# Kernel optimization log

Hardware: AMD Instinct MI355X
Metric: run time of the kernel (lower is better)

The kernel has to match this reference:

```python
import jax, jax.numpy as jnp
import numpy as np


def _lstm_scan(x_seq, W_ih, W_hh, b_ih, b_hh, hidden):
    # x_seq: [T, E]; returns final h: [1, H]. PyTorch LSTMCell gate order: i, f, g, o.
    H = hidden
    b = b_ih + b_hh  # fuse biases once

    def step(carry, x_t):
        h, c = carry  # [1, H] each
        gates = x_t[None, :] @ W_ih.T + h @ W_hh.T + b  # [1, 4H]
        i = jax.nn.sigmoid(gates[:, 0 * H:1 * H])
        f = jax.nn.sigmoid(gates[:, 1 * H:2 * H])
        g = jnp.tanh(gates[:, 2 * H:3 * H])
        o = jax.nn.sigmoid(gates[:, 3 * H:4 * H])
        c = f * c + i * g
        h = o * jnp.tanh(c)
        return (h, c), None

    h0 = jnp.zeros((1, H), dtype=x_seq.dtype)
    c0 = jnp.zeros((1, H), dtype=x_seq.dtype)
    (h, _), _ = jax.lax.scan(step, (h0, c0), x_seq)
    return h


def setup_inputs() -> dict:
    key = jax.random.key(0)
    ks = jax.random.split(key, 20)
    V_T, V_A, E, H = 50000, 20000, 1024, 2048
    T_T, T_A = 128, 16
    s = 0.02
    return {
        "x_title": jax.random.randint(ks[0], (T_T,), 0, V_T, dtype=jnp.int64) if jax.config.jax_enable_x64 else jax.random.randint(ks[0], (T_T,), 0, V_T, dtype=jnp.int32),
        "x_authors": jax.random.randint(ks[1], (T_A,), 0, V_A, dtype=jnp.int32),
        "emb_title": jax.random.normal(ks[2], (V_T, E), jnp.float32) * s,
        "emb_authors": jax.random.normal(ks[3], (V_A, E), jnp.float32) * s,
        "W_ih_t": jax.random.normal(ks[4], (4 * H, E), jnp.float32) * s,
        "W_hh_t": jax.random.normal(ks[5], (4 * H, H), jnp.float32) * s,
        "b_ih_t": jax.random.normal(ks[6], (4 * H,), jnp.float32) * s,
        "b_hh_t": jax.random.normal(ks[7], (4 * H,), jnp.float32) * s,
        "W_ih_a": jax.random.normal(ks[8], (4 * H, E), jnp.float32) * s,
        "W_hh_a": jax.random.normal(ks[9], (4 * H, H), jnp.float32) * s,
        "b_ih_a": jax.random.normal(ks[10], (4 * H,), jnp.float32) * s,
        "b_hh_a": jax.random.normal(ks[11], (4 * H,), jnp.float32) * s,
        "W1": jax.random.normal(ks[12], (H, 2 * H), jnp.float32) * s,
        "b1": jax.random.normal(ks[13], (H,), jnp.float32) * s,
        "W2": jax.random.normal(ks[14], (H, H), jnp.float32) * s,
        "b2": jax.random.normal(ks[15], (H,), jnp.float32) * s,
        "W3": jax.random.normal(ks[16], (2, H), jnp.float32) * s,
        "b3": jax.random.normal(ks[17], (2,), jnp.float32) * s,
    }


def reference(x_title, x_authors, emb_title, emb_authors,
              W_ih_t, W_hh_t, b_ih_t, b_hh_t,
              W_ih_a, W_hh_a, b_ih_a, b_hh_a,
              W1, b1, W2, b2, W3, b3):
    H = W_hh_t.shape[1]
    xt = emb_title[x_title]        # [T_t, E]
    xa = emb_authors[x_authors]    # [T_a, E]
    summary_title = _lstm_scan(xt, W_ih_t, W_hh_t, b_ih_t, b_hh_t, H)    # [1, H]
    summary_authors = _lstm_scan(xa, W_ih_a, W_hh_a, b_ih_a, b_hh_a, H)  # [1, H]
    summary = jnp.concatenate([summary_title, summary_authors], axis=1)  # [1, 2H]
    h1 = jax.nn.relu(summary @ W1.T + b1)
    h2 = jax.nn.relu(h1 @ W2.T + b2)
    logit = h2 @ W3.T + b3  # [1, 2]
    return logit
```

## Files before the change

kernel.cpp:

```cpp
#include <hip/hip_runtime.h>
#include <stdint.h>

#define NB 256
typedef unsigned long long u64;

__device__ __forceinline__ float sigm(float x) {
    return 1.f / (1.f + __expf(-x));
}
__device__ __forceinline__ float tanh_fast(float x) {
    return 1.f - 2.f / (__expf(2.f * x) + 1.f);
}

__device__ __forceinline__ u64 aload(u64* p) {
    return __hip_atomic_load(p, __ATOMIC_RELAXED, __HIP_MEMORY_SCOPE_AGENT);
}
__device__ __forceinline__ void astore(u64* p, u64 v) {
    __hip_atomic_store(p, v, __ATOMIC_RELAXED, __HIP_MEMORY_SCOPE_AGENT);
}
__device__ __forceinline__ void poll4(u64* m, unsigned tag, float* dst) {
    u64 v0, v1, v2, v3;
    for (;;) {
        v0 = aload(m + 0);
        v1 = aload(m + 1);
        v2 = aload(m + 2);
        v3 = aload(m + 3);
        if ((unsigned)(v0 >> 32) == tag && (unsigned)(v1 >> 32) == tag &&
            (unsigned)(v2 >> 32) == tag && (unsigned)(v3 >> 32) == tag)
            break;
        __builtin_amdgcn_s_sleep(1);
    }
    dst[0] = __uint_as_float((unsigned)v0);
    dst[1] = __uint_as_float((unsigned)v1);
    dst[2] = __uint_as_float((unsigned)v2);
    dst[3] = __uint_as_float((unsigned)v3);
}

template <int TT>
__global__ __launch_bounds__(256) void gates_x_gemm(
    const int* __restrict__ idx, const float* __restrict__ emb,
    const float* __restrict__ Wih, const float* __restrict__ bih,
    const float* __restrict__ bhh, float* __restrict__ Gx) {
    __shared__ float As[TT][36];
    __shared__ float Ws[32][68];
    const int tid = threadIdx.x;
    const int jt = blockIdx.x * 64;
    const int t0 = blockIdx.y * TT;
    constexpr int TPT = TT / 16;
    const int tx = tid & 15, ty = tid >> 4;
    float acc[TPT][4];
#pragma unroll
    for (int a = 0; a < TPT; ++a)
#pragma unroll
        for (int q = 0; q < 4; ++q) acc[a][q] = 0.f;

    for (int k0 = 0; k0 < 1024; k0 += 32) {
        if constexpr (TT == 32) {
            int t = tid >> 3, kq = (tid & 7) * 4;
            int row = idx[t0 + t];
            float4 v = *(const float4*)(emb + (size_t)row * 1024 + k0 + kq);
            *(float4*)&As[t][kq] = v;
        } else {
            int t = tid >> 4, kq = (tid & 15) * 2;
            int row = idx[t0 + t];
            float2 v = *(const float2*)(emb + (size_t)row * 1024 + k0 + kq);
            *(float2*)&As[t][kq] = v;
        }
        {
            int j = tid >> 3, kq = (tid & 7) * 4;
            float4 w0 = *(const float4*)(Wih + (size_t)(jt + j) * 1024 + k0 + kq);
            float4 w1 = *(const float4*)(Wih + (size_t)(jt + j + 32) * 1024 + k0 + kq);
            const float* p0 = (const float*)&w0;
            const float* p1 = (const float*)&w1;
#pragma unroll
            for (int c = 0; c < 4; ++c) {
                Ws[kq + c][j] = p0[c];
                Ws[kq + c][j + 32] = p1[c];
            }
        }
        __syncthreads();
#pragma unroll
        for (int kk = 0; kk < 32; kk += 4) {
            float4 av[TPT];
#pragma unroll
            for (int tt = 0; tt < TPT; ++tt)
                av[tt] = *(float4*)&As[ty * TPT + tt][kk];
#pragma unroll
            for (int c = 0; c < 4; ++c) {
                float4 wv = *(float4*)&Ws[kk + c][tx * 4];
#pragma unroll
                for (int tt = 0; tt < TPT; ++tt) {
                    const float* ap = (const float*)&av[tt];
                    float a = ap[c];
                    acc[tt][0] += a * wv.x;
                    acc[tt][1] += a * wv.y;
                    acc[tt][2] += a * wv.z;
                    acc[tt][3] += a * wv.w;
                }
            }
        }
        __syncthreads();
    }
    int j = jt + tx * 4;
    float4 bi = *(const float4*)(bih + j);
    float4 bh = *(const float4*)(bhh + j);
#pragma unroll
    for (int tt = 0; tt < TPT; ++tt) {
        int t = t0 + ty * TPT + tt;
        float4 r;
        r.x = acc[tt][0] + bi.x + bh.x;
        r.y = acc[tt][1] + bi.y + bh.y;
        r.z = acc[tt][2] + bi.z + bh.z;
        r.w = acc[tt][3] + bi.w + bh.w;
        *(float4*)(Gx + (size_t)t * 8192 + j) = r;
    }
}

__global__ __launch_bounds__(512, 2) void lstm_mlp_persistent(
    const float* __restrict__ Whh_t, const float* __restrict__ Whh_a,
    const float* __restrict__ Gxt, const float* __restrict__ Gxa,
    const float* __restrict__ W1, const float* __restrict__ b1,
    const float* __restrict__ W2, const float* __restrict__ b2,
    const float* __restrict__ W3, const float* __restrict__ b3,
    u64* msg_t, u64* msg_a, float* out) {
    __shared__ float h_lds[21504];
    __shared__ float part_final[32];
    __shared__ float gsum[32];
    __shared__ float cl[8];
    const int tid = threadIdx.x;
    const int b = blockIdx.x;
    const int w = tid >> 6, l = tid & 63;

    for (int scan = 0; scan < 2; ++scan) {
        const float* Whh = scan ? Whh_a : Whh_t;
        const float* Gx = scan ? Gxa : Gxt;
        u64* msg = scan ? msg_a : msg_t;
        const int T = scan ? 16 : 128;

        float4 wreg[4][8];
#pragma unroll
        for (int r = 0; r < 4; ++r) {
            const int rl = w * 4 + r;
            const int j = (rl >> 3) * 2048 + b * 8 + (rl & 7);
            const float* wrow = Whh + (size_t)j * 2048 + l * 4;
#pragma unroll
            for (int q = 0; q < 8; ++q) wreg[r][q] = *(const float4*)(wrow + q * 256);
        }
        if (tid < 8) cl[tid] = 0.f;

        for (int t = 0; t < T; ++t) {
            float gx;
            if (tid < 32)
                gx = Gx[(size_t)t * 8192 + (tid >> 3) * 2048 + b * 8 + (tid & 7)];
            if (t == 0) {
                *(float4*)(h_lds + tid * 4) = float4{0.f, 0.f, 0.f, 0.f};
            } else {
                poll4(msg + (t & 1) * 2048 + tid * 4, (unsigned)t, h_lds + tid * 4);
            }
            __syncthreads();
            float4 hreg[8];
#pragma unroll
            for (int q = 0; q < 8; ++q) hreg[q] = *(float4*)(h_lds + q * 256 + l * 4);
            float acc[4];
#pragma unroll
            for (int r = 0; r < 4; ++r) {
                float a = 0.f;
#pragma unroll
                for (int q = 0; q < 8; ++q) {
                    a += wreg[r][q].x * hreg[q].x;
                    a += wreg[r][q].y * hreg[q].y;
                    a += wreg[r][q].z * hreg[q].z;
                    a += wreg[r][q].w * hreg[q].w;
                }
                acc[r] = a;
            }
#pragma unroll
            for (int r = 0; r < 4; ++r) {
                float a = acc[r];
#pragma unroll
                for (int off = 32; off; off >>= 1) a += __shfl_xor(a, off, 64);
                if (l == 0) part_final[w * 4 + r] = a;
            }
            __syncthreads();
            if (tid < 32) gsum[tid] = part_final[tid] + gx;
            if (tid < 8) {
                float si = sigm(gsum[tid]);
                float sf = sigm(gsum[8 + tid]);
                float tg = tanh_fast(gsum[16 + tid]);
                float so = sigm(gsum[24 + tid]);
                float c = sf * cl[tid] + si * tg;
                cl[tid] = c;
                float hval = so * tanh_fast(c);
                astore(msg + ((t + 1) & 1) * 2048 + b * 8 + tid,
                       ((u64)(unsigned)(t + 1) << 32) | (u64)__float_as_uint(hval));
            }
        }
    }

    poll4(msg_t + tid * 4, 128u, h_lds + tid * 4);
    poll4(msg_a + tid * 4, 16u, h_lds + 2048 + tid * 4);
    __syncthreads();
    {
        const int j = b * 8 + w;
        const float* wr = W1 + (size_t)j * 4096;
        float acc = 0.f;
#pragma unroll
        for (int i = 0; i < 16; ++i) {
            float4 wv = *(const float4*)(wr + i * 256 + l * 4);
            float4 hv = *(const float4*)(h_lds + i * 256 + l * 4);
            acc += wv.x * hv.x + wv.y * hv.y + wv.z * hv.z + wv.w * hv.w;
        }
#pragma unroll
        for (int off = 32; off; off >>= 1) acc += __shfl_xor(acc, off, 64);
        if (l == 0) {
            float h1 = fmaxf(acc + b1[j], 0.f);
            astore(msg_t + 2048 + j, (129ull << 32) | (u64)__float_as_uint(h1));
        }
    }
    __syncthreads();
    poll4(msg_t + 2048 + tid * 4, 129u, h_lds + tid * 4);
    __syncthreads();
    {
        const int j = b * 8 + w;
        const float* wr = W2 + (size_t)j * 2048;
        float acc = 0.f;
#pragma unroll
        for (int i = 0; i < 8; ++i) {
            float4 wv = *(const float4*)(wr + i * 256 + l * 4);
            float4 hv = *(const float4*)(h_lds + i * 256 + l * 4);
            acc += wv.x * hv.x + wv.y * hv.y + wv.z * hv.z + wv.w * hv.w;
        }
#pragma unroll
        for (int off = 32; off; off >>= 1) acc += __shfl_xor(acc, off, 64);
        if (l == 0) {
            float h2 = fmaxf(acc + b2[j], 0.f);
            astore(msg_t + j, (130ull << 32) | (u64)__float_as_uint(h2));
        }
    }
    if (b == 0) {
        __syncthreads();
        poll4(msg_t + tid * 4, 130u, h_lds + tid * 4);
        __syncthreads();
        if (w < 2) {
            const float* wr = W3 + (size_t)w * 2048;
            float acc = 0.f;
#pragma unroll
            for (int i = 0; i < 8; ++i) {
                float4 wv = *(const float4*)(wr + i * 256 + l * 4);
                float4 hv = *(const float4*)(h_lds + i * 256 + l * 4);
                acc += wv.x * hv.x + wv.y * hv.y + wv.z * hv.z + wv.w * hv.w;
            }
#pragma unroll
            for (int off = 32; off; off >>= 1) acc += __shfl_xor(acc, off, 64);
            if (l == 0) out[w] = acc + b3[w];
        }
    }
}

extern "C" void kernel_launch(void* const* d_in, const int* in_sizes, int n_in,
                              void* d_out, int out_size, void* d_ws,
                              size_t ws_size, hipStream_t stream) {
    const int* x_t = (const int*)d_in[0];
    const int* x_a = (const int*)d_in[1];
    const float* emb_t = (const float*)d_in[2];
    const float* emb_a = (const float*)d_in[3];
    const float* Wih_t = (const float*)d_in[4];
    const float* Whh_t = (const float*)d_in[5];
    const float* bih_t = (const float*)d_in[6];
    const float* bhh_t = (const float*)d_in[7];
    const float* Wih_a = (const float*)d_in[8];
    const float* Whh_a = (const float*)d_in[9];
    const float* bih_a = (const float*)d_in[10];
    const float* bhh_a = (const float*)d_in[11];
    const float* W1 = (const float*)d_in[12];
    const float* b1 = (const float*)d_in[13];
    const float* W2 = (const float*)d_in[14];
    const float* b2 = (const float*)d_in[15];
    const float* W3 = (const float*)d_in[16];
    const float* b3 = (const float*)d_in[17];

    u64* msg_t = (u64*)d_ws;
    u64* msg_a = (u64*)((char*)d_ws + 32768);
    float* gxt = (float*)((char*)d_ws + 65536);
    float* gxa = (float*)((char*)d_ws + 65536 + 4194304);

    hipMemsetAsync(d_ws, 0, 65536, stream);
    gates_x_gemm<32><<<dim3(128, 4), 256, 0, stream>>>(x_t, emb_t, Wih_t, bih_t,
                                                       bhh_t, gxt);
    gates_x_gemm<16><<<dim3(128, 1), 256, 0, stream>>>(x_a, emb_a, Wih_a, bih_a,
                                                       bhh_a, gxa);
    lstm_mlp_persistent<<<NB, 512, 0, stream>>>(Whh_t, Whh_a, gxt, gxa, W1, b1,
                                                W2, b2, W3, b3, msg_t, msg_a,
                                                (float*)d_out);
}
```

Baseline: 1.200 ms.

## Map each warp to one hidden unit's four gates and drop second barrier

Row assignment now gives each wavefront the i, f, g and o rows for one hidden unit. The gate nonlinearity and cell update run in registers right after the shuffle reduction, so the per-step LDS staging and the second __syncthreads go away. The h buffer in LDS is double-buffered by step parity so the next step's poll cannot overwrite values still being read. Polling now uses two 128-bit global loads through inline asm with cache-bypass bits instead of four 64-bit atomic loads. This shortens the serial critical path per timestep, at the cost of relying on the sc0/sc1 asm for coherence and of doing redundant transcendental work across all lanes.

After: 1.163 ms. 3.0% less time.

```diff
diff --git a/kernel.cpp b/kernel.cpp
--- a/kernel.cpp
+++ b/kernel.cpp
@@ -3,6 +3,7 @@
 
 #define NB 256
 typedef unsigned long long u64;
+typedef unsigned uint4v __attribute__((ext_vector_type(4)));
 
 __device__ __forceinline__ float sigm(float x) {
     return 1.f / (1.f + __expf(-x));
@@ -11,28 +12,27 @@
     return 1.f - 2.f / (__expf(2.f * x) + 1.f);
 }
 
-__device__ __forceinline__ u64 aload(u64* p) {
-    return __hip_atomic_load(p, __ATOMIC_RELAXED, __HIP_MEMORY_SCOPE_AGENT);
-}
 __device__ __forceinline__ void astore(u64* p, u64 v) {
     __hip_atomic_store(p, v, __ATOMIC_RELAXED, __HIP_MEMORY_SCOPE_AGENT);
 }
-__device__ __forceinline__ void poll4(u64* m, unsigned tag, float* dst) {
-    u64 v0, v1, v2, v3;
+
+__device__ __forceinline__ void poll4v(const u64* m, unsigned tag, float* dst) {
+    uint4v x, y;
     for (;;) {
-        v0 = aload(m + 0);
-        v1 = aload(m + 1);
-        v2 = aload(m + 2);
-        v3 = aload(m + 3);
-        if ((unsigned)(v0 >> 32) == tag && (unsigned)(v1 >> 32) == tag &&
-            (unsigned)(v2 >> 32) == tag && (unsigned)(v3 >> 32) == tag)
-            break;
+        asm volatile(
+            "global_load_dwordx4 %0, %2, off sc0 sc1\n\t"
+            "global_load_dwordx4 %1, %3, off sc0 sc1\n\t"
+            "s_waitcnt vmcnt(0)"
+            : "=&v"(x), "=&v"(y)
+            : "v"(m), "v"(m + 2)
+            : "memory");
+        if (x.y == tag && x.w == tag && y.y == tag && y.w == tag) break;
         __builtin_amdgcn_s_sleep(1);
     }
-    dst[0] = __uint_as_float((unsigned)v0);
-    dst[1] = __uint_as_float((unsigned)v1);
-    dst[2] = __uint_as_float((unsigned)v2);
-    dst[3] = __uint_as_float((unsigned)v3);
+    dst[0] = __uint_as_float(x.x);
+    dst[1] = __uint_as_float(x.z);
+    dst[2] = __uint_as_float(y.x);
+    dst[3] = __uint_as_float(y.z);
 }
 
 template <int TT>
@@ -123,9 +123,6 @@
     const float* __restrict__ W3, const float* __restrict__ b3,
     u64* msg_t, u64* msg_a, float* out) {
     __shared__ float h_lds[21504];
-    __shared__ float part_final[32];
-    __shared__ float gsum[32];
-    __shared__ float cl[8];
     const int tid = threadIdx.x;
     const int b = blockIdx.x;
     const int w = tid >> 6, l = tid & 63;
@@ -138,66 +135,66 @@
 
         float4 wreg[4][8];
 #pragma unroll
-        for (int r = 0; r < 4; ++r) {
-            const int rl = w * 4 + r;
-            const int j = (rl >> 3) * 2048 + b * 8 + (rl & 7);
+        for (int q = 0; q < 4; ++q) {
+            const int j = q * 2048 + b * 8 + w;
             const float* wrow = Whh + (size_t)j * 2048 + l * 4;
 #pragma unroll
-            for (int q = 0; q < 8; ++q) wreg[r][q] = *(const float4*)(wrow + q * 256);
-        }
-        if (tid < 8) cl[tid] = 0.f;
+            for (int k8 = 0; k8 < 8; ++k8)
+                wreg[q][k8] = *(const float4*)(wrow + k8 * 256);
+        }
+        float c = 0.f;
 
         for (int t = 0; t < T; ++t) {
-            float gx;
-            if (tid < 32)
-                gx = Gx[(size_t)t * 8192 + (tid >> 3) * 2048 + b * 8 + (tid & 7)];
+            float gxv[4];
+#pragma unroll
+            for (int q = 0; q < 4; ++q)
+                gxv[q] = Gx[(size_t)t * 8192 + q * 2048 + b * 8 + w];
+            float* hstage = h_lds + (t & 1) * 2048;
             if (t == 0) {
-                *(float4*)(h_lds + tid * 4) = float4{0.f, 0.f, 0.f, 0.f};
+                *(float4*)(hstage + tid * 4) = float4{0.f, 0.f, 0.f, 0.f};
             } else {
-                poll4(msg + (t & 1) * 2048 + tid * 4, (unsigned)t, h_lds + tid * 4);
+                poll4v(msg + (t & 1) * 2048 + tid * 4, (unsigned)t,
+                       hstage + tid * 4);
             }
             __syncthreads();
             float4 hreg[8];
 #pragma unroll
-            for (int q = 0; q < 8; ++q) hreg[q] = *(float4*)(h_lds + q * 256 + l * 4);
+            for (int k8 = 0; k8 < 8; ++k8)
+                hreg[k8] = *(float4*)(hstage + k8 * 256 + l * 4);
             float acc[4];
 #pragma unroll
-            for (int r = 0; r < 4; ++r) {
+            for (int q = 0; q < 4; ++q) {
                 float a = 0.f;
 #pragma unroll
-                for (int q = 0; q < 8; ++q) {
-                    a += wreg[r][q].x * hreg[q].x;
-                    a += wreg[r][q].y * hreg[q].y;
-                    a += wreg[r][q].z * hreg[q].z;
-                    a += wreg[r][q].w * hreg[q].w;
+                for (int k8 = 0; k8 < 8; ++k8) {
+                    a += wreg[q][k8].x * hreg[k8].x;
+                    a += wreg[q][k8].y * hreg[k8].y;
+                    a += wreg[q][k8].z * hreg[k8].z;
+                    a += wreg[q][k8].w * hreg[k8].w;
                 }
-                acc[r] = a;
-            }
-#pragma unroll
-            for (int r = 0; r < 4; ++r) {
-                float a = acc[r];
+                acc[q] = a;
+            }
+#pragma unroll
+            for (int q = 0; q < 4; ++q) {
+                float a = acc[q];
 #pragma unroll
                 for (int off = 32; off; off >>= 1) a += __shfl_xor(a, off, 64);
-                if (l == 0) part_final[w * 4 + r] = a;
-            }
-            __syncthreads();
-            if (tid < 32) gsum[tid] = part_final[tid] + gx;
-            if (tid < 8) {
-                float si = sigm(gsum[tid]);
-                float sf = sigm(gsum[8 + tid]);
-                float tg = tanh_fast(gsum[16 + tid]);
-                float so = sigm(gsum[24 + tid]);
-                float c = sf * cl[tid] + si * tg;
-                cl[tid] = c;
-                float hval = so * tanh_fast(c);
-                astore(msg + ((t + 1) & 1) * 2048 + b * 8 + tid,
+                acc[q] = a;
+            }
+            float gi = sigm(acc[0] + gxv[0]);
+            float gf = sigm(acc[1] + gxv[1]);
+            float gg = tanh_fast(acc[2] + gxv[2]);
+            float go = sigm(acc[3] + gxv[3]);
+            c = gf * c + gi * gg;
+            float hval = go * tanh_fast(c);
+            if (l == 0)
+                astore(msg + ((t + 1) & 1) * 2048 + b * 8 + w,
                        ((u64)(unsigned)(t + 1) << 32) | (u64)__float_as_uint(hval));
-            }
-        }
-    }
-
-    poll4(msg_t + tid * 4, 128u, h_lds + tid * 4);
-    poll4(msg_a + tid * 4, 16u, h_lds + 2048 + tid * 4);
+        }
+    }
+
+    poll4v(msg_t + tid * 4, 128u, h_lds + tid * 4);
+    poll4v(msg_a + tid * 4, 16u, h_lds + 2048 + tid * 4);
     __syncthreads();
     {
         const int j = b * 8 + w;
@@ -217,7 +214,7 @@
         }
     }
     __syncthreads();
-    poll4(msg_t + 2048 + tid * 4, 129u, h_lds + tid * 4);
+    poll4v(msg_t + 2048 + tid * 4, 129u, h_lds + tid * 4);
     __syncthreads();
     {
         const int j = b * 8 + w;
@@ -238,7 +235,7 @@
     }
     if (b == 0) {
         __syncthreads();
-        poll4(msg_t + tid * 4, 130u, h_lds + tid * 4);
+        poll4v(msg_t + tid * 4, 130u, h_lds + tid * 4);
         __syncthreads();
         if (w < 2) {
             const float* wr = W3 + (size_t)w * 2048;
```
